# Kernel optimization log

Measured on AMD Instinct MI355X. Metric: run time of the kernel, lower is better.

The kernel has to match this reference:

```python
import jax, jax.numpy as jnp
import numpy as np

B, S, I, H = 64, 2048, 64, 128


def setup_inputs() -> dict:
    key = jax.random.key(0)
    ks = jax.random.split(key, 4)
    return {
        'x': jax.random.normal(ks[0], (B, S, I), dtype=jnp.float32),
        'w0': jax.random.normal(ks[1], (I, H), dtype=jnp.float32) * 0.1,
        'u0': jax.random.normal(ks[2], (H, H), dtype=jnp.float32) * 0.1,
        'bg0': jnp.ones((1, H), jnp.float32),
        'bu0': jnp.ones((1, H), jnp.float32),
        'zeta0': jnp.full((1, 1), 1.0, jnp.float32),
        'nu0': jnp.full((1, 1), -4.0, jnp.float32),
        'lambd0': jnp.zeros((1,), jnp.float32),
        'gamma0': jnp.full((1,), 0.999, jnp.float32),
        'w1': jax.random.normal(jax.random.fold_in(key, 10), (H, H), dtype=jnp.float32) * 0.1,
        'u1': jax.random.normal(ks[3], (H, H), dtype=jnp.float32) * 0.1,
        'bg1': jnp.ones((1, H), jnp.float32),
        'bu1': jnp.ones((1, H), jnp.float32),
        'zeta1': jnp.full((1, 1), 1.0, jnp.float32),
        'nu1': jnp.full((1, 1), -4.0, jnp.float32),
        'lambd1': jnp.zeros((1,), jnp.float32),
        'gamma1': jnp.full((1,), 0.999, jnp.float32),
    }


def _layer(x_seq, w, u, bg, bu, zeta, nu, lambd, gamma):
    # x_seq: [B, S, in]; precompute input projection for all timesteps
    wx = jnp.einsum('bsi,ih->bsh', x_seq, w)  # [B, S, H]
    sz = jax.nn.sigmoid(zeta)  # [1,1]
    sn = jax.nn.sigmoid(nu)    # [1,1]
    gc = jnp.clip(gamma, 0.0, 1.0)  # [1]
    h0 = jnp.zeros((x_seq.shape[0], u.shape[0]), x_seq.dtype)

    def step(h, wx_t):
        pre = wx_t + h @ u            # [B, H]
        z = jax.nn.sigmoid(pre + bg)  # gate
        h_hat = jnp.tanh(pre + bu)    # update
        h_new = z * h + (sz * (1.0 - z) + sn) * h_hat
        h_comfi = gc * h_new + (1.0 - gc) * lambd
        return h_comfi, h_comfi

    h_T, outs = jax.lax.scan(step, h0, jnp.swapaxes(wx, 0, 1))  # outs: [S, B, H]
    return jnp.swapaxes(outs, 0, 1), h_T


def reference(x, w0, u0, bg0, bu0, zeta0, nu0, lambd0, gamma0,
              w1, u1, bg1, bu1, zeta1, nu1, lambd1, gamma1):
    out0, h0T = _layer(x, w0, u0, bg0, bu0, zeta0, nu0, lambd0, gamma0)
    out1, h1T = _layer(out0, w1, u1, bg1, bu1, zeta1, nu1, lambd1, gamma1)
    h_n = jnp.stack([h0T, h1T], axis=0)  # [num_layers, B, H]
    return out1, h_n
```

## Files before the change

kernel.cpp:

```cpp
#include <hip/hip_runtime.h>
#include <hip/hip_bf16.h>

#define BB 64
#define SS 2048
#define II 64
#define HH 128
#define CH 64

typedef _Float16 half8 __attribute__((ext_vector_type(8)));
typedef float f32x4 __attribute__((ext_vector_type(4)));
struct u64x2 { unsigned long long x, y; };

#define LOG2E 1.44269504088896340736f

__device__ __forceinline__ float sigm(float x) { return 1.0f / (1.0f + __expf(-x)); }

__global__ __launch_bounds__(256, 4)
void wx0_kernel(const float* __restrict__ x, const float* __restrict__ w0,
                float* __restrict__ wx0) {
  __shared__ float xs[32][64];
  const int tid = threadIdx.x;
  const int j = tid & (HH - 1);
  const int rh = tid >> 7;
  const long row0 = (long)blockIdx.x * 32;

  float w0c[II];
#pragma unroll
  for (int i = 0; i < II; ++i) w0c[i] = w0[i * HH + j];

  const float4* xg = (const float4*)(x + row0 * II);
  float4* xsv = (float4*)&xs[0][0];
  xsv[tid] = xg[tid];
  xsv[tid + 256] = xg[tid + 256];
  __syncthreads();

#pragma unroll
  for (int rp = 0; rp < 16; ++rp) {
    int r = rp * 2 + rh;
    float acc = 0.f;
#pragma unroll
    for (int i = 0; i < II; i += 4) {
      float4 xv = *(const float4*)&xs[r][i];
      acc += w0c[i] * xv.x + w0c[i + 1] * xv.y + w0c[i + 2] * xv.z +
             w0c[i + 3] * xv.w;
    }
    wx0[(row0 + r) * HH + j] = acc;
  }
}

__global__ __launch_bounds__(256, 1)
void scan_kernel(const float* __restrict__ wx0,
                 const float* __restrict__ u0, const float* __restrict__ bg0,
                 const float* __restrict__ bu0, const float* __restrict__ zeta0,
                 const float* __restrict__ nu0, const float* __restrict__ lambd0,
                 const float* __restrict__ gamma0,
                 const float* __restrict__ w1, const float* __restrict__ u1,
                 const float* __restrict__ bg1, const float* __restrict__ bu1,
                 const float* __restrict__ zeta1, const float* __restrict__ nu1,
                 const float* __restrict__ lambd1, const float* __restrict__ gamma1,
                 float* __restrict__ out1, float* __restrict__ hn) {
  const int b = blockIdx.x;
  const int tid = threadIdx.x;
  const int w = tid >> 6;
  const int l = tid & 63;
  const int g = l >> 4;
  const int n = l & 15;
  const int c0 = 32 * w + n;
  const int c1 = c0 + 16;
  const bool L1 = (g == 1);

  const float* Wm0 = u0; const float* Wm1 = w1; const float* Wm2 = u1;
  half8 wf[3][2][4];
#pragma unroll
  for (int mt = 0; mt < 3; ++mt) {
    const float* W = (mt == 0) ? Wm0 : (mt == 1) ? Wm1 : Wm2;
#pragma unroll
    for (int nt = 0; nt < 2; ++nt) {
      const int col = 32 * w + 16 * nt + n;
#pragma unroll
      for (int kt = 0; kt < 4; ++kt) {
        half8 f;
#pragma unroll
        for (int i = 0; i < 8; ++i) {
          int k = 32 * kt + (i < 4 ? 4 * g + i : 16 + 4 * g + (i - 4));
          f[i] = (_Float16)W[k * HH + col];
        }
        wf[mt][nt][kt] = f;
      }
    }
  }

  const float szg = L1 ? sigm(zeta1[0]) : sigm(zeta0[0]);
  const float sng = L1 ? sigm(nu1[0]) : sigm(nu0[0]);
  const float gcr = L1 ? gamma1[0] : gamma0[0];
  const float gcg = fminf(fmaxf(gcr, 0.f), 1.f);
  const float kcg = (1.f - gcg) * (L1 ? lambd1[0] : lambd0[0]);
  const float ebg_0 = -LOG2E * (L1 ? bg1[c0] : bg0[c0]);
  const float ebg_1 = -LOG2E * (L1 ? bg1[c1] : bg0[c1]);
  const float ebu_0 = -2.f * LOG2E * (L1 ? bu1[c0] : bu0[c0]);
  const float ebu_1 = -2.f * LOG2E * (L1 ? bu1[c1] : bu0[c1]);

  auto gate = [&](float pre, float hp, float eg, float eu) -> float {
    float p  = __builtin_amdgcn_exp2f(__builtin_fmaf(pre, -LOG2E, eg));
    float qq = __builtin_amdgcn_exp2f(__builtin_fmaf(pre, -2.f * LOG2E, eu));
    float opp = 1.f + p, opq = 1.f + qq, omq = 1.f - qq;
    float t1 = __builtin_fmaf(sng, opp, szg * p);
    float num = __builtin_fmaf(hp, opq, t1 * omq);
    float hnew = num * __builtin_amdgcn_rcpf(opp * opq);
    return __builtin_fmaf(gcg, hnew, kcg);
  };

  __shared__ __align__(16) _Float16 Hs[2][2][HH];
  __shared__ __align__(16) float wxb[CH * HH];

  const float* wxg = wx0 + (size_t)b * SS * HH;
  float* outg = out1 + (size_t)b * SS * HH;

  {
    const float4* src = (const float4*)(wxg + HH);
    float4* dst = (float4*)wxb;
#pragma unroll
    for (int i = 0; i < 8; ++i) dst[i * 256 + tid] = src[i * 256 + tid];
  }
  float h_prev0, h_prev1;
  {
    float pr0 = wxg[c0], pr1 = wxg[c1];
    float h00 = gate(pr0, 0.f, ebg_0, ebu_0);
    float h01 = gate(pr1, 0.f, ebg_1, ebu_1);
    h_prev0 = (g == 0) ? h00 : 0.f;
    h_prev1 = (g == 0) ? h01 : 0.f;
    if (g == 0) { Hs[0][0][c0] = (_Float16)h00; Hs[0][0][c1] = (_Float16)h01; }
    if (g == 1) { Hs[0][1][c0] = (_Float16)0.f; Hs[0][1][c1] = (_Float16)0.f; }
  }
  asm volatile("s_waitcnt lgkmcnt(0)" ::: "memory");
  __builtin_amdgcn_s_barrier();

  half8 a0[4], a1[4];
#pragma unroll
  for (int kt = 0; kt < 4; ++kt) { a0[kt] = (half8)(_Float16)0.f; a1[kt] = (half8)(_Float16)0.f; }

  const f32x4 zero = {0.f, 0.f, 0.f, 0.f};

  for (int t = 0; t < SS; ++t) {
    const int rd = t & 1, wr = rd ^ 1;
    const int q = t & (CH - 1);

    if (n == 0) {
      const _Float16* h0r = &Hs[rd][0][0];
      const _Float16* h1r = &Hs[rd][1][0];
#pragma unroll
      for (int kt = 0; kt < 4; ++kt) {
        u64x2 t0 = { *(const unsigned long long*)(h0r + 32 * kt + 4 * g),
                     *(const unsigned long long*)(h0r + 32 * kt + 16 + 4 * g) };
        a0[kt] = __builtin_bit_cast(half8, t0);
        u64x2 t1v = { *(const unsigned long long*)(h1r + 32 * kt + 4 * g),
                      *(const unsigned long long*)(h1r + 32 * kt + 16 + 4 * g) };
        a1[kt] = __builtin_bit_cast(half8, t1v);
      }
    }

    float wxv0 = wxb[q * HH + c0];
    float wxv1 = wxb[q * HH + c1];

    f32x4 accA0, accA1, accB0, accB1, accC0, accC1;
#pragma unroll
    for (int kt = 0; kt < 4; ++kt) {
      accA0 = __builtin_amdgcn_mfma_f32_16x16x32_f16(a0[kt], wf[0][0][kt], kt ? accA0 : zero, 0, 0, 0);
      accA1 = __builtin_amdgcn_mfma_f32_16x16x32_f16(a0[kt], wf[0][1][kt], kt ? accA1 : zero, 0, 0, 0);
      accB0 = __builtin_amdgcn_mfma_f32_16x16x32_f16(a0[kt], wf[1][0][kt], kt ? accB0 : zero, 0, 0, 0);
      accB1 = __builtin_amdgcn_mfma_f32_16x16x32_f16(a0[kt], wf[1][1][kt], kt ? accB1 : zero, 0, 0, 0);
      accC0 = __builtin_amdgcn_mfma_f32_16x16x32_f16(a1[kt], wf[2][0][kt], kt ? accC0 : zero, 0, 0, 0);
      accC1 = __builtin_amdgcn_mfma_f32_16x16x32_f16(a1[kt], wf[2][1][kt], kt ? accC1 : zero, 0, 0, 0);
    }

    float s0 = accB0[0] + accC0[0];
    float s1 = accB1[0] + accC1[0];
    float sw0 = __int_as_float(__builtin_amdgcn_ds_swizzle(__float_as_int(s0), 0x401F));
    float sw1 = __int_as_float(__builtin_amdgcn_ds_swizzle(__float_as_int(s1), 0x401F));

    float pre0 = (g == 0) ? accA0[0] + wxv0 : sw0;
    float pre1 = (g == 0) ? accA1[0] + wxv1 : sw1;

    float hc0 = gate(pre0, h_prev0, ebg_0, ebu_0);
    float hc1 = gate(pre1, h_prev1, ebg_1, ebu_1);

    if (g < 2) {
      Hs[wr][g][c0] = (_Float16)hc0;
      Hs[wr][g][c1] = (_Float16)hc1;
    }
    if (g == 1) {
      outg[(size_t)t * HH + c0] = hc0;
      outg[(size_t)t * HH + c1] = hc1;
    }
    if (t == SS - 2 && g == 0) {
      hn[b * HH + c0] = hc0;
      hn[b * HH + c1] = hc1;
    }
    if (t == SS - 1 && g == 1) {
      hn[BB * HH + b * HH + c0] = hc0;
      hn[BB * HH + b * HH + c1] = hc1;
    }
    h_prev0 = hc0;
    h_prev1 = hc1;

    asm volatile("s_waitcnt lgkmcnt(0)" ::: "memory");
    __builtin_amdgcn_s_barrier();

    if (q == CH - 1 && t + 1 < SS) {
      float4* wdst = (float4*)wxb;
#pragma unroll
      for (int i = 0; i < 8; ++i) {
        int flat4 = i * 256 + tid;
        int row = t + 2 + (flat4 >> 5);
        row = row < SS ? row : SS - 1;
        int col4 = flat4 & 31;
        wdst[flat4] = *(const float4*)(wxg + (size_t)row * HH + col4 * 4);
      }
      asm volatile("s_waitcnt lgkmcnt(0)" ::: "memory");
      __builtin_amdgcn_s_barrier();
    }
  }
}

extern "C" void kernel_launch(void* const* d_in, const int* in_sizes, int n_in,
                              void* d_out, int out_size, void* d_ws, size_t ws_size,
                              hipStream_t stream) {
  const float* x      = (const float*)d_in[0];
  const float* w0     = (const float*)d_in[1];
  const float* u0     = (const float*)d_in[2];
  const float* bg0    = (const float*)d_in[3];
  const float* bu0    = (const float*)d_in[4];
  const float* zeta0  = (const float*)d_in[5];
  const float* nu0    = (const float*)d_in[6];
  const float* lambd0 = (const float*)d_in[7];
  const float* gamma0 = (const float*)d_in[8];
  const float* w1     = (const float*)d_in[9];
  const float* u1     = (const float*)d_in[10];
  const float* bg1    = (const float*)d_in[11];
  const float* bu1    = (const float*)d_in[12];
  const float* zeta1  = (const float*)d_in[13];
  const float* nu1    = (const float*)d_in[14];
  const float* lambd1 = (const float*)d_in[15];
  const float* gamma1 = (const float*)d_in[16];

  float* out = (float*)d_out;
  float* hn  = out + (size_t)BB * SS * HH;
  float* wx0 = (float*)d_ws;

  wx0_kernel<<<(BB * SS) / 32, 256, 0, stream>>>(x, w0, wx0);
  scan_kernel<<<BB, 256, 0, stream>>>(wx0, u0, bg0, bu0, zeta0, nu0, lambd0,
                                      gamma0, w1, u1, bg1, bu1, zeta1, nu1,
                                      lambd1, gamma1, out, hn);
}
```

Baseline: 920.0 us.

## Pack hidden state for direct MFMA operand loads and unchain MFMA accumulation

Replaces the per-layer fp16 hidden-state buffer with a packed layout whose 8-element groups match the MFMA A-operand K ordering, so every lane can load its operand with one 16-byte LDS read. The previous path had only lane n==0 gather it. The four K-step MFMAs per output tile now use independent zero accumulators and are summed afterward, which shortens the serial MFMA dependency chain. The ds_swizzle cross-group transfer is dropped: all four lane groups now do gate work, split by layer parity and column half. The cost is more MFMA result registers, extra adds, and redundant LDS reads across lanes.

```diff
diff --git a/kernel.cpp b/kernel.cpp
--- a/kernel.cpp
+++ b/kernel.cpp
@@ -9,7 +9,6 @@
 
 typedef _Float16 half8 __attribute__((ext_vector_type(8)));
 typedef float f32x4 __attribute__((ext_vector_type(4)));
-struct u64x2 { unsigned long long x, y; };
 
 #define LOG2E 1.44269504088896340736f
 
@@ -67,13 +66,13 @@
   const int n = l & 15;
   const int c0 = 32 * w + n;
   const int c1 = c0 + 16;
-  const bool L1 = (g == 1);
-
-  const float* Wm0 = u0; const float* Wm1 = w1; const float* Wm2 = u1;
+  const int parity = g & 1;
+  const int colsel = g >> 1;
+
   half8 wf[3][2][4];
 #pragma unroll
   for (int mt = 0; mt < 3; ++mt) {
-    const float* W = (mt == 0) ? Wm0 : (mt == 1) ? Wm1 : Wm2;
+    const float* W = (mt == 0) ? u0 : (mt == 1) ? w1 : u1;
 #pragma unroll
     for (int nt = 0; nt < 2; ++nt) {
       const int col = 32 * w + 16 * nt + n;
@@ -90,31 +89,35 @@
     }
   }
 
-  const float szg = L1 ? sigm(zeta1[0]) : sigm(zeta0[0]);
-  const float sng = L1 ? sigm(nu1[0]) : sigm(nu0[0]);
-  const float gcr = L1 ? gamma1[0] : gamma0[0];
-  const float gcg = fminf(fmaxf(gcr, 0.f), 1.f);
-  const float kcg = (1.f - gcg) * (L1 ? lambd1[0] : lambd0[0]);
-  const float ebg_0 = -LOG2E * (L1 ? bg1[c0] : bg0[c0]);
-  const float ebg_1 = -LOG2E * (L1 ? bg1[c1] : bg0[c1]);
-  const float ebu_0 = -2.f * LOG2E * (L1 ? bu1[c0] : bu0[c0]);
-  const float ebu_1 = -2.f * LOG2E * (L1 ? bu1[c1] : bu0[c1]);
-
-  auto gate = [&](float pre, float hp, float eg, float eu) -> float {
+  const float szg = parity ? sigm(zeta1[0]) : sigm(zeta0[0]);
+  const float sng = parity ? sigm(nu1[0]) : sigm(nu0[0]);
+  const float gcraw = parity ? gamma1[0] : gamma0[0];
+  const float gcg = fminf(fmaxf(gcraw, 0.f), 1.f);
+  const float kcg = (1.f - gcg) * (parity ? lambd1[0] : lambd0[0]);
+  const float ebg_0 = -LOG2E * (parity ? bg1[c0] : bg0[c0]);
+  const float ebg_1 = -LOG2E * (parity ? bg1[c1] : bg0[c1]);
+  const float ebu_0 = -2.f * LOG2E * (parity ? bu1[c0] : bu0[c0]);
+  const float ebu_1 = -2.f * LOG2E * (parity ? bu1[c1] : bu0[c1]);
+
+  auto gate = [](float pre, float hp, float eg, float eu, float sz, float sn,
+                 float gc, float kc) -> float {
     float p  = __builtin_amdgcn_exp2f(__builtin_fmaf(pre, -LOG2E, eg));
     float qq = __builtin_amdgcn_exp2f(__builtin_fmaf(pre, -2.f * LOG2E, eu));
     float opp = 1.f + p, opq = 1.f + qq, omq = 1.f - qq;
-    float t1 = __builtin_fmaf(sng, opp, szg * p);
+    float t1 = __builtin_fmaf(sn, opp, sz * p);
     float num = __builtin_fmaf(hp, opq, t1 * omq);
     float hnew = num * __builtin_amdgcn_rcpf(opp * opq);
-    return __builtin_fmaf(gcg, hnew, kcg);
+    return __builtin_fmaf(gc, hnew, kc);
   };
 
-  __shared__ __align__(16) _Float16 Hs[2][2][HH];
+  __shared__ __align__(16) _Float16 Hpk[2][2][160];
   __shared__ __align__(16) float wxb[CH * HH];
 
   const float* wxg = wx0 + (size_t)b * SS * HH;
   float* outg = out1 + (size_t)b * SS * HH;
+
+  const int widx = (w * 4 + (n >> 2)) * 8 + (n & 3) + (colsel << 2);
+  const int rbase = 8 * g;
 
   {
     const float4* src = (const float4*)(wxg + HH);
@@ -122,22 +125,22 @@
 #pragma unroll
     for (int i = 0; i < 8; ++i) dst[i * 256 + tid] = src[i * 256 + tid];
   }
-  float h_prev0, h_prev1;
+  float hp0, hp1;
   {
-    float pr0 = wxg[c0], pr1 = wxg[c1];
-    float h00 = gate(pr0, 0.f, ebg_0, ebu_0);
-    float h01 = gate(pr1, 0.f, ebg_1, ebu_1);
-    h_prev0 = (g == 0) ? h00 : 0.f;
-    h_prev1 = (g == 0) ? h01 : 0.f;
-    if (g == 0) { Hs[0][0][c0] = (_Float16)h00; Hs[0][0][c1] = (_Float16)h01; }
-    if (g == 1) { Hs[0][1][c0] = (_Float16)0.f; Hs[0][1][c1] = (_Float16)0.f; }
+    const float sz0 = sigm(zeta0[0]), sn0 = sigm(nu0[0]);
+    const float gc0 = fminf(fmaxf(gamma0[0], 0.f), 1.f);
+    const float kc0 = (1.f - gc0) * lambd0[0];
+    float h00 = gate(wxg[c0], 0.f, -LOG2E * bg0[c0], -2.f * LOG2E * bu0[c0],
+                     sz0, sn0, gc0, kc0);
+    float h01 = gate(wxg[c1], 0.f, -LOG2E * bg0[c1], -2.f * LOG2E * bu0[c1],
+                     sz0, sn0, gc0, kc0);
+    hp0 = parity ? 0.f : h00;
+    hp1 = parity ? 0.f : h01;
+    float wv = parity ? 0.f : (colsel ? h01 : h00);
+    Hpk[0][parity][widx] = (_Float16)wv;
   }
   asm volatile("s_waitcnt lgkmcnt(0)" ::: "memory");
   __builtin_amdgcn_s_barrier();
-
-  half8 a0[4], a1[4];
-#pragma unroll
-  for (int kt = 0; kt < 4; ++kt) { a0[kt] = (half8)(_Float16)0.f; a1[kt] = (half8)(_Float16)0.f; }
 
   const f32x4 zero = {0.f, 0.f, 0.f, 0.f};
 
@@ -145,63 +148,49 @@
     const int rd = t & 1, wr = rd ^ 1;
     const int q = t & (CH - 1);
 
-    if (n == 0) {
-      const _Float16* h0r = &Hs[rd][0][0];
-      const _Float16* h1r = &Hs[rd][1][0];
-#pragma unroll
-      for (int kt = 0; kt < 4; ++kt) {
-        u64x2 t0 = { *(const unsigned long long*)(h0r + 32 * kt + 4 * g),
-                     *(const unsigned long long*)(h0r + 32 * kt + 16 + 4 * g) };
-        a0[kt] = __builtin_bit_cast(half8, t0);
-        u64x2 t1v = { *(const unsigned long long*)(h1r + 32 * kt + 4 * g),
-                      *(const unsigned long long*)(h1r + 32 * kt + 16 + 4 * g) };
-        a1[kt] = __builtin_bit_cast(half8, t1v);
-      }
-    }
-
+    half8 a0[4], a1[4];
+#pragma unroll
+    for (int kt = 0; kt < 4; ++kt) {
+      a0[kt] = __builtin_bit_cast(half8,
+                 *(const uint4*)&Hpk[rd][0][kt * 32 + rbase]);
+      a1[kt] = __builtin_bit_cast(half8,
+                 *(const uint4*)&Hpk[rd][1][kt * 32 + rbase]);
+    }
     float wxv0 = wxb[q * HH + c0];
     float wxv1 = wxb[q * HH + c1];
 
-    f32x4 accA0, accA1, accB0, accB1, accC0, accC1;
+    f32x4 A0[4], A1[4], B0[4], B1[4], C0[4], C1[4];
 #pragma unroll
     for (int kt = 0; kt < 4; ++kt) {
-      accA0 = __builtin_amdgcn_mfma_f32_16x16x32_f16(a0[kt], wf[0][0][kt], kt ? accA0 : zero, 0, 0, 0);
-      accA1 = __builtin_amdgcn_mfma_f32_16x16x32_f16(a0[kt], wf[0][1][kt], kt ? accA1 : zero, 0, 0, 0);
-      accB0 = __builtin_amdgcn_mfma_f32_16x16x32_f16(a0[kt], wf[1][0][kt], kt ? accB0 : zero, 0, 0, 0);
-      accB1 = __builtin_amdgcn_mfma_f32_16x16x32_f16(a0[kt], wf[1][1][kt], kt ? accB1 : zero, 0, 0, 0);
-      accC0 = __builtin_amdgcn_mfma_f32_16x16x32_f16(a1[kt], wf[2][0][kt], kt ? accC0 : zero, 0, 0, 0);
-      accC1 = __builtin_amdgcn_mfma_f32_16x16x32_f16(a1[kt], wf[2][1][kt], kt ? accC1 : zero, 0, 0, 0);
-    }
-
-    float s0 = accB0[0] + accC0[0];
-    float s1 = accB1[0] + accC1[0];
-    float sw0 = __int_as_float(__builtin_amdgcn_ds_swizzle(__float_as_int(s0), 0x401F));
-    float sw1 = __int_as_float(__builtin_amdgcn_ds_swizzle(__float_as_int(s1), 0x401F));
-
-    float pre0 = (g == 0) ? accA0[0] + wxv0 : sw0;
-    float pre1 = (g == 0) ? accA1[0] + wxv1 : sw1;
-
-    float hc0 = gate(pre0, h_prev0, ebg_0, ebu_0);
-    float hc1 = gate(pre1, h_prev1, ebg_1, ebu_1);
-
-    if (g < 2) {
-      Hs[wr][g][c0] = (_Float16)hc0;
-      Hs[wr][g][c1] = (_Float16)hc1;
-    }
-    if (g == 1) {
-      outg[(size_t)t * HH + c0] = hc0;
-      outg[(size_t)t * HH + c1] = hc1;
-    }
-    if (t == SS - 2 && g == 0) {
-      hn[b * HH + c0] = hc0;
-      hn[b * HH + c1] = hc1;
-    }
-    if (t == SS - 1 && g == 1) {
-      hn[BB * HH + b * HH + c0] = hc0;
-      hn[BB * HH + b * HH + c1] = hc1;
-    }
-    h_prev0 = hc0;
-    h_prev1 = hc1;
+      A0[kt] = __builtin_amdgcn_mfma_f32_16x16x32_f16(a0[kt], wf[0][0][kt], zero, 0, 0, 0);
+      A1[kt] = __builtin_amdgcn_mfma_f32_16x16x32_f16(a0[kt], wf[0][1][kt], zero, 0, 0, 0);
+      B0[kt] = __builtin_amdgcn_mfma_f32_16x16x32_f16(a0[kt], wf[1][0][kt], zero, 0, 0, 0);
+      B1[kt] = __builtin_amdgcn_mfma_f32_16x16x32_f16(a0[kt], wf[1][1][kt], zero, 0, 0, 0);
+      C0[kt] = __builtin_amdgcn_mfma_f32_16x16x32_f16(a1[kt], wf[2][0][kt], zero, 0, 0, 0);
+      C1[kt] = __builtin_amdgcn_mfma_f32_16x16x32_f16(a1[kt], wf[2][1][kt], zero, 0, 0, 0);
+    }
+    float sumA0 = (A0[0][0] + A0[1][0]) + (A0[2][0] + A0[3][0]);
+    float sumA1 = (A1[0][0] + A1[1][0]) + (A1[2][0] + A1[3][0]);
+    float sumB0 = (B0[0][0] + B0[1][0]) + (B0[2][0] + B0[3][0]);
+    float sumB1 = (B1[0][0] + B1[1][0]) + (B1[2][0] + B1[3][0]);
+    float sumC0 = (C0[0][0] + C0[1][0]) + (C0[2][0] + C0[3][0]);
+    float sumC1 = (C1[0][0] + C1[1][0]) + (C1[2][0] + C1[3][0]);
+
+    float pre_0 = parity ? (sumB0 + sumC0) : (sumA0 + wxv0);
+    float pre_1 = parity ? (sumB1 + sumC1) : (sumA1 + wxv1);
+    float hc0 = gate(pre_0, hp0, ebg_0, ebu_0, szg, sng, gcg, kcg);
+    float hc1 = gate(pre_1, hp1, ebg_1, ebu_1, szg, sng, gcg, kcg);
+    hp0 = hc0;
+    hp1 = hc1;
+
+    float wval = colsel ? hc1 : hc0;
+    Hpk[wr][parity][widx] = (_Float16)wval;
+    if (parity) {
+      outg[(size_t)t * HH + (colsel ? c1 : c0)] = wval;
+      if (t == SS - 1) hn[BB * HH + b * HH + (colsel ? c1 : c0)] = wval;
+    } else {
+      if (t == SS - 2) hn[b * HH + (colsel ? c1 : c0)] = wval;
+    }
 
     asm volatile("s_waitcnt lgkmcnt(0)" ::: "memory");
     __builtin_amdgcn_s_barrier();
```

New measurement: 1.230 ms. +33.7%, slower.
